# Performance work log

Measured on AMD Instinct MI355X. Metric: run time of the kernel, lower is better.

## Reference

```python
import jax, jax.numpy as jnp
import numpy as np

N = 100000   # nodes
E = 1600000  # edges
IN, H, OUT = 128, 128, 40
BN_EPS = 1e-5


def setup_inputs() -> dict:
    key = jax.random.key(0)
    ks = jax.random.split(key, 8)
    x = jax.random.normal(ks[0], (N, IN), jnp.float32)
    edge_src = jax.random.randint(ks[1], (E,), 0, N, jnp.int32)
    edge_dst = jax.random.randint(ks[2], (E,), 0, N, jnp.int32)

    def glorot(k, shape):
        lim = (6.0 / (shape[0] + shape[1])) ** 0.5
        return jax.random.uniform(k, shape, jnp.float32, -lim, lim)

    return {
        "x": x, "edge_src": edge_src, "edge_dst": edge_dst,
        "W1": glorot(ks[3], (IN, H)), "b1": jnp.zeros((H,), jnp.float32),
        "g1": jnp.ones((H,), jnp.float32), "bt1": jnp.zeros((H,), jnp.float32),
        "W2": glorot(ks[4], (H, H)), "b2": jnp.zeros((H,), jnp.float32),
        "g2": jnp.ones((H,), jnp.float32), "bt2": jnp.zeros((H,), jnp.float32),
        "Wr": glorot(ks[5], (H, OUT)), "br": jnp.zeros((OUT,), jnp.float32),
    }


def _gcn_conv(h_in, W, b, src, dst, dinv):
    # GCNConv: D^{-1/2}(A+I)D^{-1/2} X W + b  (symmetric norm w/ self-loops)
    h = h_in @ W                                   # [N,H]
    coef = dinv[src] * dinv[dst]                   # [E]
    agg = jax.ops.segment_sum(h[src] * coef[:, None], dst, num_segments=N)
    agg = agg + h * (dinv * dinv)[:, None]         # self-loop contribution
    return agg + b


def _bn_relu(h, gamma, beta):
    # BatchNorm1d in training mode (batch stats, biased variance) + ReLU
    mean = jnp.mean(h, axis=0)
    var = jnp.var(h, axis=0)
    y = (h - mean) * jax.lax.rsqrt(var + BN_EPS) * gamma + beta
    return jax.nn.relu(y)


def reference(x, edge_src, edge_dst, W1, b1, g1, bt1, W2, b2, g2, bt2, Wr, br):
    ones = jnp.ones((E,), jnp.float32)
    deg = jax.ops.segment_sum(ones, edge_dst, num_segments=N) + 1.0  # +1 self-loop
    dinv = jax.lax.rsqrt(deg)

    h = _gcn_conv(x, W1, b1, edge_src, edge_dst, dinv)
    h = _bn_relu(h, g1, bt1)
    h = _gcn_conv(h, W2, b2, edge_src, edge_dst, dinv)
    h = _bn_relu(h, g2, bt2)
    # dropout omitted (deterministic eval); readout linear
    return h @ Wr + br
```

## Files before the change

kernel.cpp:

```cpp
#include <hip/hip_runtime.h>
#include <hip/hip_bf16.h>
#include <hip/hip_fp16.h>

#define H_DIM 128

typedef _Float16 half8 __attribute__((ext_vector_type(8)));
typedef float floatx4 __attribute__((ext_vector_type(4)));

__global__ void degree_kernel(const int* __restrict__ dst, int* __restrict__ deg, int E_) {
    int i = blockIdx.x * blockDim.x + threadIdx.x;
    if (i < E_) atomicAdd(&deg[dst[i]], 1);
}

__global__ void scan_block_kernel(const int* __restrict__ deg, float* __restrict__ dinv,
                                  int* __restrict__ rowptr, int* __restrict__ bsum, int N_) {
    __shared__ int sh[256];
    int i = blockIdx.x * 256 + threadIdx.x;
    int v = (i < N_) ? deg[i] : 0;
    if (i < N_) dinv[i] = rsqrtf((float)v + 1.0f);
    sh[threadIdx.x] = v;
    __syncthreads();
    for (int off = 1; off < 256; off <<= 1) {
        int t = (threadIdx.x >= off) ? sh[threadIdx.x - off] : 0;
        __syncthreads();
        sh[threadIdx.x] += t;
        __syncthreads();
    }
    if (i < N_) rowptr[i] = sh[threadIdx.x] - v;
    if (threadIdx.x == 255) bsum[blockIdx.x] = sh[255];
}

__global__ void scan_add_kernel(int* __restrict__ rowptr, const int* __restrict__ bsum,
                                int N_, int E_) {
    __shared__ int red[256];
    const int b = blockIdx.x, t = threadIdx.x;
    int s = 0;
    for (int j = t; j < b; j += 256) s += bsum[j];
    red[t] = s;
    __syncthreads();
    for (int off = 128; off > 0; off >>= 1) {
        if (t < off) red[t] += red[t + off];
        __syncthreads();
    }
    int boff = red[0];
    int i = b * 256 + t;
    if (i < N_) rowptr[i] += boff;
    if (i == 0) rowptr[N_] = E_;
}

__global__ void csr_fill_kernel(const int* __restrict__ src, const int* __restrict__ dst,
                                const int* __restrict__ rowptr, int* __restrict__ cursor,
                                int* __restrict__ cols, int E_, int N_, int shift) {
    int b = blockIdx.x & 7;
    if (((N_ - 1) >> shift) < b) return;
    int i = (blockIdx.x >> 3) * blockDim.x + threadIdx.x;
    if (i < E_) {
        int d = dst[i];
        if ((d >> shift) == b) {
            int p = rowptr[d] + atomicAdd(&cursor[d], 1);
            cols[p] = src[i];
        }
    }
}

__device__ inline half8 a_frag_f32(const float* Xr, int k0) {
    float4 v0 = *(const float4*)(Xr + k0);
    float4 v1 = *(const float4*)(Xr + k0 + 4);
    half8 a;
    a[0] = (_Float16)v0.x; a[1] = (_Float16)v0.y; a[2] = (_Float16)v0.z; a[3] = (_Float16)v0.w;
    a[4] = (_Float16)v1.x; a[5] = (_Float16)v1.y; a[6] = (_Float16)v1.z; a[7] = (_Float16)v1.w;
    return a;
}
__device__ inline half8 a_frag_f16_bn(const _Float16* Xr, int k0,
                                      const float* A, const float* B) {
    half8 r = *(const half8*)(Xr + k0);
    float4 a0 = *(const float4*)(A + k0);
    float4 a1 = *(const float4*)(A + k0 + 4);
    float4 b0 = *(const float4*)(B + k0);
    float4 b1 = *(const float4*)(B + k0 + 4);
    half8 o;
    o[0] = (_Float16)fmaxf(fmaf((float)r[0], a0.x, b0.x), 0.f);
    o[1] = (_Float16)fmaxf(fmaf((float)r[1], a0.y, b0.y), 0.f);
    o[2] = (_Float16)fmaxf(fmaf((float)r[2], a0.z, b0.z), 0.f);
    o[3] = (_Float16)fmaxf(fmaf((float)r[3], a0.w, b0.w), 0.f);
    o[4] = (_Float16)fmaxf(fmaf((float)r[4], a1.x, b1.x), 0.f);
    o[5] = (_Float16)fmaxf(fmaf((float)r[5], a1.y, b1.y), 0.f);
    o[6] = (_Float16)fmaxf(fmaf((float)r[6], a1.z, b1.z), 0.f);
    o[7] = (_Float16)fmaxf(fmaf((float)r[7], a1.w, b1.w), 0.f);
    return o;
}

template<bool BN, typename InT>
__global__ __launch_bounds__(256) void gemm_mfma_kernel(
    const InT* __restrict__ X, const float* __restrict__ W,
    const float* __restrict__ gsum, const float* __restrict__ gsq,
    const float* __restrict__ gamma, const float* __restrict__ beta,
    const float* __restrict__ dinv,
    _Float16* __restrict__ Y, int N_)
{
    __shared__ _Float16 Wf[32 * 64 * 8];
    __shared__ __align__(16) float Alds[128], Blds[128];

    const int tid = threadIdx.x;
    if constexpr (BN) {
        if (tid < 128) {
            float inv_n = 1.0f / (float)N_;
            float mean = gsum[tid] * inv_n;
            float var  = gsq[tid] * inv_n - mean * mean;
            float a = rsqrtf(var + 1e-5f) * gamma[tid];
            Alds[tid] = a;
            Blds[tid] = beta[tid] - mean * a;
        }
    }
    for (int idx = tid; idx < 128 * 32; idx += 256) {
        int k = idx >> 5;
        int n0 = (idx & 31) * 4;
        float4 w = *(const float4*)(W + k * 128 + n0);
        int kb = k >> 5, q = (k >> 3) & 3, j = k & 7;
#pragma unroll
        for (int u = 0; u < 4; ++u) {
            int n = n0 + u;
            int lane = (n & 15) | (q << 4);
            Wf[((((n >> 4) * 4 + kb) * 64 + lane) << 3) + j] = (_Float16)((&w.x)[u]);
        }
    }
    __syncthreads();

    const int wv = tid >> 6, lane = tid & 63;
    const int m = lane & 15, q = lane >> 4;
    const int row0 = blockIdx.x * 64 + wv * 16;

    int arow = row0 + m;
    if (arow >= N_) arow = N_ - 1;
    const InT* Xr = X + (size_t)arow * H_DIM;

    half8 a[4];
#pragma unroll
    for (int kb = 0; kb < 4; ++kb) {
        int k0 = kb * 32 + q * 8;
        if constexpr (BN) a[kb] = a_frag_f16_bn((const _Float16*)Xr, k0, Alds, Blds);
        else              a[kb] = a_frag_f32((const float*)Xr, k0);
    }

    floatx4 acc[8];
#pragma unroll
    for (int nt = 0; nt < 8; ++nt) acc[nt] = (floatx4){0.f, 0.f, 0.f, 0.f};

#pragma unroll
    for (int nt = 0; nt < 8; ++nt) {
#pragma unroll
        for (int kb = 0; kb < 4; ++kb) {
            half8 b = *(const half8*)&Wf[(((nt * 4 + kb) * 64 + lane) << 3)];
            acc[nt] = __builtin_amdgcn_mfma_f32_16x16x32_f16(a[kb], b, acc[nt], 0, 0, 0);
        }
    }

#pragma unroll
    for (int r = 0; r < 4; ++r) {
        int row = row0 + q * 4 + r;
        if (row < N_) {
            float ds = dinv[row];
            _Float16* Yr = Y + (size_t)row * H_DIM + m;
#pragma unroll
            for (int nt = 0; nt < 8; ++nt)
                Yr[nt * 16] = (_Float16)(ds * acc[nt][r]);
        }
    }
}

__global__ __launch_bounds__(256) void readout_mfma_kernel(
    const _Float16* __restrict__ X, const float* __restrict__ W,
    const float* __restrict__ gsum, const float* __restrict__ gsq,
    const float* __restrict__ gamma, const float* __restrict__ beta,
    const float* __restrict__ br,
    float* __restrict__ Y, int N_, int OUTC)
{
    __shared__ _Float16 Wf[12 * 64 * 8];
    __shared__ __align__(16) float Alds[128], Blds[128];

    const int tid = threadIdx.x;
    if (tid < 128) {
        float inv_n = 1.0f / (float)N_;
        float mean = gsum[tid] * inv_n;
        float var  = gsq[tid] * inv_n - mean * mean;
        float a = rsqrtf(var + 1e-5f) * gamma[tid];
        Alds[tid] = a;
        Blds[tid] = beta[tid] - mean * a;
    }
    for (int idx = tid; idx < 128 * 64; idx += 256) {
        int k = idx >> 6, n = idx & 63;
        if (n < 48) {
            float w = (n < OUTC) ? W[k * OUTC + n] : 0.f;
            int kb = k >> 5, q = (k >> 3) & 3, j = k & 7;
            int lane = (n & 15) | (q << 4);
            Wf[((((n >> 4) * 4 + kb) * 64 + lane) << 3) + j] = (_Float16)w;
        }
    }
    __syncthreads();

    const int wv = tid >> 6, lane = tid & 63;
    const int m = lane & 15, q = lane >> 4;
    const int row0 = blockIdx.x * 64 + wv * 16;

    int arow = row0 + m;
    if (arow >= N_) arow = N_ - 1;
    const _Float16* Xr = X + (size_t)arow * H_DIM;

    half8 a[4];
#pragma unroll
    for (int kb = 0; kb < 4; ++kb)
        a[kb] = a_frag_f16_bn(Xr, kb * 32 + q * 8, Alds, Blds);

    floatx4 acc[3];
#pragma unroll
    for (int nt = 0; nt < 3; ++nt) acc[nt] = (floatx4){0.f, 0.f, 0.f, 0.f};

#pragma unroll
    for (int nt = 0; nt < 3; ++nt) {
#pragma unroll
        for (int kb = 0; kb < 4; ++kb) {
            half8 b = *(const half8*)&Wf[(((nt * 4 + kb) * 64 + lane) << 3)];
            acc[nt] = __builtin_amdgcn_mfma_f32_16x16x32_f16(a[kb], b, acc[nt], 0, 0, 0);
        }
    }

#pragma unroll
    for (int nt = 0; nt < 3; ++nt) {
        int col = nt * 16 + m;
        if (col < OUTC) {
            float bb = br[col];
#pragma unroll
            for (int r = 0; r < 4; ++r) {
                int row = row0 + q * 4 + r;
                if (row < N_)
                    Y[(size_t)row * OUTC + col] = acc[nt][r] + bb;
            }
        }
    }
}

__global__ __launch_bounds__(256) void aggregate_stats_kernel(
    const __half2* __restrict__ Gp,
    const int* __restrict__ rowptr,
    const int* __restrict__ cols,
    const float* __restrict__ dinv, const float* __restrict__ bias,
    __half2* __restrict__ out,
    float* __restrict__ gsum, float* __restrict__ gsq,
    int N_, int stride)
{
    const int wave = threadIdx.x >> 6;
    const int lane = threadIdx.x & 63;
    const int c2 = lane * 2;
    const float bs0 = bias[c2], bs1 = bias[c2 + 1];
    const __half2 z = __float2half2_rn(0.f);

    float r0 = 0.f, r1 = 0.f, q0 = 0.f, q1 = 0.f;

    const int n0 = blockIdx.x * 4 + wave;
    int e0 = 0, e1 = 0, f0 = 0, f1 = 0;
    int c[24];
    if (n0 < N_) {
        e0 = rowptr[n0]; e1 = rowptr[n0 + 1];
        int n1 = n0 + stride; if (n1 > N_ - 1) n1 = N_ - 1;
        f0 = rowptr[n1]; f1 = rowptr[n1 + 1];
#pragma unroll
        for (int u = 0; u < 24; ++u) {
            int ee = e0 + u;
            c[u] = (e1 > e0) ? cols[ee < e1 ? ee : e1 - 1] : 0;
        }
    }

    for (int n = n0; n < N_; n += stride) {
        __half2 self = Gp[((unsigned)n << 6) | (unsigned)lane];
        __half2 h[24];
#pragma unroll
        for (int u = 0; u < 24; ++u)
            h[u] = Gp[((unsigned)c[u] << 6) | (unsigned)lane];

        int n2 = n + 2 * stride; if (n2 > N_ - 1) n2 = N_ - 1;
        int g0 = rowptr[n2], g1 = rowptr[n2 + 1];

        {
            int ff0 = f0, ff1 = f1;
#pragma unroll
            for (int u = 0; u < 24; ++u) {
                int ee = ff0 + u;
                c[u] = (ff1 > ff0) ? cols[ee < ff1 ? ee : ff1 - 1] : 0;
            }
        }

        __half2 acc[8];
        acc[0] = self;
#pragma unroll
        for (int u = 1; u < 8; ++u) acc[u] = z;
#pragma unroll
        for (int u = 0; u < 24; ++u)
            acc[u & 7] = __hadd2(acc[u & 7], (e0 + u < e1) ? h[u] : z);

        for (int e = e0 + 24; e < e1; e += 8) {
            int cc[8];
#pragma unroll
            for (int u = 0; u < 8; ++u) { int ee = e + u; cc[u] = cols[ee < e1 ? ee : e1 - 1]; }
#pragma unroll
            for (int u = 0; u < 8; ++u) h[u] = Gp[((unsigned)cc[u] << 6) | (unsigned)lane];
#pragma unroll
            for (int u = 0; u < 8; ++u) acc[u] = __hadd2(acc[u], (e + u < e1) ? h[u] : z);
        }

        __half2 p0 = __hadd2(__hadd2(acc[0], acc[1]), __hadd2(acc[2], acc[3]));
        __half2 p1 = __hadd2(__hadd2(acc[4], acc[5]), __hadd2(acc[6], acc[7]));
        float2 F0 = __half22float2(p0);
        float2 F1 = __half22float2(p1);
        float di = dinv[n];
        float o0 = fmaf(di, F0.x + F1.x, bs0);
        float o1 = fmaf(di, F0.y + F1.y, bs1);
        out[((unsigned)n << 6) | (unsigned)lane] = __floats2half2_rn(o0, o1);

        r0 += o0; r1 += o1;
        q0 = fmaf(o0, o0, q0); q1 = fmaf(o1, o1, q1);

        e0 = f0; e1 = f1; f0 = g0; f1 = g1;
    }

    __shared__ float ssum[4][128], ssq[4][128];
    ssum[wave][c2] = r0; ssum[wave][c2 + 1] = r1;
    ssq[wave][c2]  = q0; ssq[wave][c2 + 1]  = q1;
    __syncthreads();
    if (threadIdx.x < 128) {
        int k = threadIdx.x;
        float s = (ssum[0][k] + ssum[1][k]) + (ssum[2][k] + ssum[3][k]);
        float q = (ssq[0][k] + ssq[1][k]) + (ssq[2][k] + ssq[3][k]);
        atomicAdd(&gsum[k], s);
        atomicAdd(&gsq[k], q);
    }
}

extern "C" void kernel_launch(void* const* d_in, const int* in_sizes, int n_in,
                              void* d_out, int out_size, void* d_ws, size_t ws_size,
                              hipStream_t stream) {
    const float* x   = (const float*)d_in[0];
    const int* esrc  = (const int*)d_in[1];
    const int* edst  = (const int*)d_in[2];
    const float* W1  = (const float*)d_in[3];
    const float* b1  = (const float*)d_in[4];
    const float* g1  = (const float*)d_in[5];
    const float* bt1 = (const float*)d_in[6];
    const float* W2  = (const float*)d_in[7];
    const float* b2  = (const float*)d_in[8];
    const float* g2  = (const float*)d_in[9];
    const float* bt2 = (const float*)d_in[10];
    const float* Wr  = (const float*)d_in[11];
    const float* br  = (const float*)d_in[12];

    const int N_ = in_sizes[0] / H_DIM;
    const int E_ = in_sizes[1];
    const int OUTC = out_size / N_;

    char* p = (char*)d_ws;
    auto alloc = [&](size_t bytes) -> void* {
        void* r = (void*)p;
        p += (bytes + 255) & ~(size_t)255;
        return r;
    };
    __half* tmpA = (__half*)alloc((size_t)N_ * H_DIM * 2);
    __half* tmpB = (__half*)alloc((size_t)N_ * H_DIM * 2);
    int*   cols  = (int*)  alloc((size_t)E_ * 4);
    int*   rowptr= (int*)  alloc((size_t)(N_ + 1) * 4);
    size_t degcur_sz = ((size_t)2 * N_ * 4 + 255) & ~(size_t)255;
    int*   degcur= (int*)  alloc((size_t)2 * N_ * 4);
    float* bnbuf = (float*)alloc(8 * 128 * 4);
    int*   deg   = degcur;
    int*   cursor= degcur + N_;
    float* sum1 = bnbuf,       *sq1 = bnbuf + 128;
    float* sum2 = bnbuf + 256, *sq2 = bnbuf + 384;
    float* dinv  = (float*)alloc((size_t)N_ * 4);
    int*   bsum  = (int*)  alloc(4096);

    hipMemsetAsync(degcur, 0, degcur_sz + 4 * 128 * 4, stream);

    const int nb = (N_ + 255) / 256;
    const int eb = (E_ + 255) / 256;
    const int ntiles64 = (N_ + 63) / 64;

    int shift = 0;
    while (((N_ - 1) >> shift) > 7) ++shift;

    const int AGG_BLOCKS = 2048;
    const int AGG_STRIDE = AGG_BLOCKS * 4;

    degree_kernel<<<eb, 256, 0, stream>>>(edst, deg, E_);
    scan_block_kernel<<<nb, 256, 0, stream>>>(deg, dinv, rowptr, bsum, N_);
    scan_add_kernel<<<nb, 256, 0, stream>>>(rowptr, bsum, N_, E_);
    csr_fill_kernel<<<eb * 8, 256, 0, stream>>>(esrc, edst, rowptr, cursor, cols, E_, N_, shift);

    gemm_mfma_kernel<false, float><<<ntiles64, 256, 0, stream>>>(
        x, W1, nullptr, nullptr, nullptr, nullptr, dinv, (_Float16*)tmpA, N_);
    aggregate_stats_kernel<<<AGG_BLOCKS, 256, 0, stream>>>(
        (const __half2*)tmpA, rowptr, cols, dinv, b1, (__half2*)tmpB,
        sum1, sq1, N_, AGG_STRIDE);

    gemm_mfma_kernel<true, _Float16><<<ntiles64, 256, 0, stream>>>(
        (const _Float16*)tmpB, W2, sum1, sq1, g1, bt1, dinv, (_Float16*)tmpA, N_);
    aggregate_stats_kernel<<<AGG_BLOCKS, 256, 0, stream>>>(
        (const __half2*)tmpA, rowptr, cols, dinv, b2, (__half2*)tmpB,
        sum2, sq2, N_, AGG_STRIDE);

    readout_mfma_kernel<<<ntiles64, 256, 0, stream>>>(
        (const _Float16*)tmpB, Wr, sum2, sq2, g2, bt2, br, (float*)d_out, N_, OUTC);
}
```

Baseline: 517.5 us.

## Pad CSR rows to multiples of 8 with zero-row sentinel to drop bounds checks

```diff
diff --git a/kernel.cpp b/kernel.cpp
--- a/kernel.cpp
+++ b/kernel.cpp
@@ -6,6 +6,8 @@
 
 typedef _Float16 half8 __attribute__((ext_vector_type(8)));
 typedef float floatx4 __attribute__((ext_vector_type(4)));
+
+__device__ inline int imax(int a, int b) { return a > b ? a : b; }
 
 __global__ void degree_kernel(const int* __restrict__ dst, int* __restrict__ deg, int E_) {
     int i = blockIdx.x * blockDim.x + threadIdx.x;
@@ -18,7 +20,8 @@
     int i = blockIdx.x * 256 + threadIdx.x;
     int v = (i < N_) ? deg[i] : 0;
     if (i < N_) dinv[i] = rsqrtf((float)v + 1.0f);
-    sh[threadIdx.x] = v;
+    int pd = (i < N_) ? imax(24, (v + 7) & ~7) : 0;
+    sh[threadIdx.x] = pd;
     __syncthreads();
     for (int off = 1; off < 256; off <<= 1) {
         int t = (threadIdx.x >= off) ? sh[threadIdx.x - off] : 0;
@@ -26,12 +29,12 @@
         sh[threadIdx.x] += t;
         __syncthreads();
     }
-    if (i < N_) rowptr[i] = sh[threadIdx.x] - v;
+    if (i < N_) rowptr[i] = sh[threadIdx.x] - pd;
     if (threadIdx.x == 255) bsum[blockIdx.x] = sh[255];
 }
 
 __global__ void scan_add_kernel(int* __restrict__ rowptr, const int* __restrict__ bsum,
-                                int N_, int E_) {
+                                const int* __restrict__ deg, int* __restrict__ cols, int N_) {
     __shared__ int red[256];
     const int b = blockIdx.x, t = threadIdx.x;
     int s = 0;
@@ -44,8 +47,15 @@
     }
     int boff = red[0];
     int i = b * 256 + t;
-    if (i < N_) rowptr[i] += boff;
-    if (i == 0) rowptr[N_] = E_;
+    if (i < N_) {
+        int start = rowptr[i] + boff;
+        rowptr[i] = start;
+        int d = deg[i];
+        int pd = imax(24, (d + 7) & ~7);
+        int padv = N_ << 8;
+        for (int j = start + d; j < start + pd; ++j) cols[j] = padv;
+        if (i == N_ - 1) rowptr[N_] = start + pd;
+    }
 }
 
 __global__ void csr_fill_kernel(const int* __restrict__ src, const int* __restrict__ dst,
@@ -58,7 +68,7 @@
         int d = dst[i];
         if ((d >> shift) == b) {
             int p = rowptr[d] + atomicAdd(&cursor[d], 1);
-            cols[p] = src[i];
+            cols[p] = src[i] << 8;
         }
     }
 }
@@ -252,6 +262,8 @@
     const int lane = threadIdx.x & 63;
     const int c2 = lane * 2;
     const float bs0 = bias[c2], bs1 = bias[c2 + 1];
+    const char* gpb = (const char*)Gp;
+    const unsigned lane4 = (unsigned)lane * 4u;
     const __half2 z = __float2half2_rn(0.f);
 
     float r0 = 0.f, r1 = 0.f, q0 = 0.f, q1 = 0.f;
@@ -260,34 +272,28 @@
     int e0 = 0, e1 = 0, f0 = 0, f1 = 0;
     int c[24];
     if (n0 < N_) {
-        e0 = rowptr[n0]; e1 = rowptr[n0 + 1];
+        e0 = __builtin_amdgcn_readfirstlane(rowptr[n0]);
+        e1 = __builtin_amdgcn_readfirstlane(rowptr[n0 + 1]);
         int n1 = n0 + stride; if (n1 > N_ - 1) n1 = N_ - 1;
-        f0 = rowptr[n1]; f1 = rowptr[n1 + 1];
-#pragma unroll
-        for (int u = 0; u < 24; ++u) {
-            int ee = e0 + u;
-            c[u] = (e1 > e0) ? cols[ee < e1 ? ee : e1 - 1] : 0;
-        }
+        f0 = __builtin_amdgcn_readfirstlane(rowptr[n1]);
+        f1 = __builtin_amdgcn_readfirstlane(rowptr[n1 + 1]);
+#pragma unroll
+        for (int u = 0; u < 24; ++u) c[u] = cols[e0 + u];
     }
 
     for (int n = n0; n < N_; n += stride) {
-        __half2 self = Gp[((unsigned)n << 6) | (unsigned)lane];
+        __half2 self = *(const __half2*)(gpb + (((unsigned)n << 8) + lane4));
         __half2 h[24];
 #pragma unroll
         for (int u = 0; u < 24; ++u)
-            h[u] = Gp[((unsigned)c[u] << 6) | (unsigned)lane];
+            h[u] = *(const __half2*)(gpb + ((unsigned)c[u] + lane4));
 
         int n2 = n + 2 * stride; if (n2 > N_ - 1) n2 = N_ - 1;
-        int g0 = rowptr[n2], g1 = rowptr[n2 + 1];
-
-        {
-            int ff0 = f0, ff1 = f1;
-#pragma unroll
-            for (int u = 0; u < 24; ++u) {
-                int ee = ff0 + u;
-                c[u] = (ff1 > ff0) ? cols[ee < ff1 ? ee : ff1 - 1] : 0;
-            }
-        }
+        int g0 = __builtin_amdgcn_readfirstlane(rowptr[n2]);
+        int g1 = __builtin_amdgcn_readfirstlane(rowptr[n2 + 1]);
+
+#pragma unroll
+        for (int u = 0; u < 24; ++u) c[u] = cols[f0 + u];
 
         __half2 acc[8];
         acc[0] = self;
@@ -295,16 +301,15 @@
         for (int u = 1; u < 8; ++u) acc[u] = z;
 #pragma unroll
         for (int u = 0; u < 24; ++u)
-            acc[u & 7] = __hadd2(acc[u & 7], (e0 + u < e1) ? h[u] : z);
+            acc[u & 7] = __hadd2(acc[u & 7], h[u]);
 
         for (int e = e0 + 24; e < e1; e += 8) {
-            int cc[8];
-#pragma unroll
-            for (int u = 0; u < 8; ++u) { int ee = e + u; cc[u] = cols[ee < e1 ? ee : e1 - 1]; }
-#pragma unroll
-            for (int u = 0; u < 8; ++u) h[u] = Gp[((unsigned)cc[u] << 6) | (unsigned)lane];
-#pragma unroll
-            for (int u = 0; u < 8; ++u) acc[u] = __hadd2(acc[u], (e + u < e1) ? h[u] : z);
+            __half2 t[8];
+#pragma unroll
+            for (int u = 0; u < 8; ++u)
+                t[u] = *(const __half2*)(gpb + ((unsigned)cols[e + u] + lane4));
+#pragma unroll
+            for (int u = 0; u < 8; ++u) acc[u] = __hadd2(acc[u], t[u]);
         }
 
         __half2 p0 = __hadd2(__hadd2(acc[0], acc[1]), __hadd2(acc[2], acc[3]));
@@ -314,7 +319,7 @@
         float di = dinv[n];
         float o0 = fmaf(di, F0.x + F1.x, bs0);
         float o1 = fmaf(di, F0.y + F1.y, bs1);
-        out[((unsigned)n << 6) | (unsigned)lane] = __floats2half2_rn(o0, o1);
+        out[((size_t)n << 6) + lane] = __floats2half2_rn(o0, o1);
 
         r0 += o0; r1 += o1;
         q0 = fmaf(o0, o0, q0); q1 = fmaf(o1, o1, q1);
@@ -362,9 +367,9 @@
         p += (bytes + 255) & ~(size_t)255;
         return r;
     };
-    __half* tmpA = (__half*)alloc((size_t)N_ * H_DIM * 2);
-    __half* tmpB = (__half*)alloc((size_t)N_ * H_DIM * 2);
-    int*   cols  = (int*)  alloc((size_t)E_ * 4);
+    __half* tmpA = (__half*)alloc((size_t)(N_ + 1) * H_DIM * 2);
+    __half* tmpB = (__half*)alloc((size_t)(N_ + 1) * H_DIM * 2);
+    int*   cols  = (int*)  alloc(((size_t)E_ + 31 * (size_t)N_ + 64) * 4);
     int*   rowptr= (int*)  alloc((size_t)(N_ + 1) * 4);
     size_t degcur_sz = ((size_t)2 * N_ * 4 + 255) & ~(size_t)255;
     int*   degcur= (int*)  alloc((size_t)2 * N_ * 4);
@@ -377,6 +382,8 @@
     int*   bsum  = (int*)  alloc(4096);
 
     hipMemsetAsync(degcur, 0, degcur_sz + 4 * 128 * 4, stream);
+    hipMemsetAsync(tmpA + (size_t)N_ * H_DIM, 0, H_DIM * 2, stream);
+    hipMemsetAsync(tmpB + (size_t)N_ * H_DIM, 0, H_DIM * 2, stream);
 
     const int nb = (N_ + 255) / 256;
     const int eb = (E_ + 255) / 256;
@@ -390,7 +397,7 @@
 
     degree_kernel<<<eb, 256, 0, stream>>>(edst, deg, E_);
     scan_block_kernel<<<nb, 256, 0, stream>>>(deg, dinv, rowptr, bsum, N_);
-    scan_add_kernel<<<nb, 256, 0, stream>>>(rowptr, bsum, N_, E_);
+    scan_add_kernel<<<nb, 256, 0, stream>>>(rowptr, bsum, deg, cols, N_);
     csr_fill_kernel<<<eb * 8, 256, 0, stream>>>(esrc, edst, rowptr, cursor, cols, E_, N_, shift);
 
     gemm_mfma_kernel<false, float><<<ntiles64, 256, 0, stream>>>(
```

After: 509.2 us. No clear change (-1.6%).
